# Kernel optimization log

Hardware: AMD Instinct MI355X
Metric: run time of the kernel (lower is better)

Reference implementation:

```python
import jax, jax.numpy as jnp
import numpy as np

ALPHA = 1.0   # get_spike_fn('ArcTan', 1.0, 20.0)
WIDTH = 20.0

@jax.custom_vjp
def arctan_spike(x):
    # Heaviside forward, ArcTan surrogate gradient
    return (x > 0).astype(x.dtype)

def _spike_fwd(x):
    return arctan_spike(x), x

def _spike_bwd(x, g):
    return (g * ALPHA / (1.0 + (WIDTH * x) ** 2),)

arctan_spike.defvjp(_spike_fwd, _spike_bwd)

T, B, F = 2048, 64, 512  # seq_len, batch, features (input_groups=256 -> F=512)
TAU_SYN, TAU_MEM, V_THRESH, W_SCALE = 0.08, 0.03, 1.0, 0.4

def setup_inputs() -> dict:
    key = jax.random.key(0)
    x = jax.random.normal(key, (T, B, F), dtype=jnp.float32)
    # ff weight: block_diag of input_groups copies of 0.4*I2 == 0.4*I_F
    W = (W_SCALE * jnp.eye(F, dtype=jnp.float32))
    leak_i = jnp.full((F,), 1.0 - TAU_SYN, dtype=jnp.float32)
    leak_v = jnp.full((F,), 1.0 - TAU_MEM, dtype=jnp.float32)
    thresh = jnp.full((F,), V_THRESH, dtype=jnp.float32)
    return {"x": x, "W": W, "leak_i": leak_i, "leak_v": leak_v, "thresh": thresh}

def reference(x, W, leak_i, leak_v, thresh):
    Tn, Bn, Fn = x.shape
    i0 = jnp.zeros((Bn, Fn), dtype=x.dtype)
    v0 = jnp.zeros((Bn, Fn), dtype=x.dtype)
    z0 = jnp.zeros((Bn, Fn), dtype=x.dtype)

    def step(carry, xt):
        i, v, z = carry
        ff = xt @ W.T                      # [B,F] linear synapse (no bias)
        i_new = leak_i * i + ff            # leaky synaptic current
        v_new = leak_v * v * (1.0 - z) + i_new  # membrane, reset-to-zero on spike
        z_new = arctan_spike(v_new - thresh)
        return (i_new, v_new, z_new), z_new

    _, out = jax.lax.scan(step, (i0, v0, z0), x)
    return out  # [T, B, F]
```

## Files before the change

### kernel.cpp

```cpp
#include <hip/hip_runtime.h>


typedef float v2f __attribute__((ext_vector_type(2)));
typedef float v4f __attribute__((ext_vector_type(4)));

constexpr int T_STEPS = 2048;
constexpr int B_DIM   = 64;
constexpr int F_DIM   = 512;
constexpr int BF      = B_DIM * F_DIM;
constexpr int BLK_FLOATS = 128;
constexpr int NBLK    = BF / BLK_FLOATS;
constexpr int CHUNK   = 64;
constexpr int NCHUNK  = T_STEPS / CHUNK;
constexpr int NPROD   = 4;
constexpr int STEPS_PER_PROD = CHUNK / NPROD;
constexpr int LOADS_PER_PROD = STEPS_PER_PROD / 2;
constexpr int LDS_FLOATS = 2 * CHUNK * BLK_FLOATS;

__global__ __launch_bounds__(320, 1) void snn_scan_kernel(
    const float* __restrict__ x,
    const float* __restrict__ W,
    const float* __restrict__ leak_i,
    const float* __restrict__ leak_v,
    const float* __restrict__ thresh,
    float* __restrict__ out) {

    __shared__ float lds[LDS_FLOATS];

    const int tid  = threadIdx.x;
    const int wid  = tid >> 6;
    const int lane = tid & 63;
    const int blk  = blockIdx.x;
    const bool is_prod = (wid < NPROD);

    const int  half = lane >> 5;
    const int  l32  = lane & 31;
    const int  sbase = wid * STEPS_PER_PROD + half;
    const float* xsrc = x + (size_t)blk * BLK_FLOATS + (size_t)l32 * 4;

    const int e  = blk * BLK_FLOATS + lane * 2;
    const int f0 = e & (F_DIM - 1);
    float w00 = 0.f, w01 = 0.f, w10 = 0.f, w11 = 0.f;
    float li0 = 0.f, li1 = 0.f, lv0 = 0.f, lv1 = 0.f, th0 = 0.f, th1 = 0.f;
    if (!is_prod) {
        w00 = W[(size_t)(f0    ) * F_DIM + f0    ];
        w01 = W[(size_t)(f0    ) * F_DIM + f0 + 1];
        w10 = W[(size_t)(f0 + 1) * F_DIM + f0    ];
        w11 = W[(size_t)(f0 + 1) * F_DIM + f0 + 1];
        li0 = leak_i[f0]; li1 = leak_i[f0 + 1];
        lv0 = leak_v[f0]; lv1 = leak_v[f0 + 1];
        th0 = thresh[f0]; th1 = thresh[f0 + 1];
    }
    float i0 = 0.f, v0 = 0.f, z0 = 0.f;
    float i1 = 0.f, v1 = 0.f, z1 = 0.f;
    float* osrc = out + e;

    auto produce = [&](int c) {
        const int db = c & 1;
        const float* gb = xsrc + (size_t)(c * CHUNK + sbase) * BF;
        v4f r[LOADS_PER_PROD];
        #pragma unroll
        for (int i = 0; i < LOADS_PER_PROD; ++i)
            r[i] = __builtin_nontemporal_load(
                       (const v4f*)(gb + (size_t)(2 * i) * BF));
        float* lb = &lds[(size_t)db * (CHUNK * BLK_FLOATS)
                         + (size_t)sbase * BLK_FLOATS + (size_t)l32 * 4];
        #pragma unroll
        for (int i = 0; i < LOADS_PER_PROD; ++i)
            *(v4f*)(lb + (size_t)(2 * i) * BLK_FLOATS) = r[i];
    };

    auto consume = [&](int c) {
        const int db = c & 1;
        const float* lb = &lds[(size_t)db * (CHUNK * BLK_FLOATS) + (size_t)lane * 2];
        float* ob = osrc + (size_t)c * CHUNK * BF;
        #pragma unroll 8
        for (int j = 0; j < CHUNK; ++j) {
            const v2f xv = *(const v2f*)(lb + (size_t)j * BLK_FLOATS);
            const float xe = xv.x;
            const float xo = xv.y;
            const float ff0 = __fadd_rn(__fmul_rn(w00, xe), __fmul_rn(w01, xo));
            const float ff1 = __fadd_rn(__fmul_rn(w10, xe), __fmul_rn(w11, xo));
            i0 = __fadd_rn(__fmul_rn(li0, i0), ff0);
            i1 = __fadd_rn(__fmul_rn(li1, i1), ff1);
            float vm0 = __fmul_rn(lv0, v0);
            float vm1 = __fmul_rn(lv1, v1);
            vm0 = (z0 > 0.0f) ? 0.0f : vm0;
            vm1 = (z1 > 0.0f) ? 0.0f : vm1;
            v0 = __fadd_rn(vm0, i0);
            v1 = __fadd_rn(vm1, i1);
            z0 = (v0 > th0) ? 1.0f : 0.0f;
            z1 = (v1 > th1) ? 1.0f : 0.0f;
            v2f zv; zv.x = z0; zv.y = z1;
            __builtin_nontemporal_store(zv, (v2f*)(ob + (size_t)j * BF));
        }
    };

    if (is_prod) produce(0);
    __syncthreads();

    for (int c = 0; c < NCHUNK; ++c) {
        if (is_prod) {
            if (c + 1 < NCHUNK) produce(c + 1);
        } else {
            consume(c);
        }
        __syncthreads();
    }
}

extern "C" void kernel_launch(void* const* d_in, const int* in_sizes, int n_in,
                              void* d_out, int out_size, void* d_ws, size_t ws_size,
                              hipStream_t stream) {
    const float* x      = (const float*)d_in[0];
    const float* W      = (const float*)d_in[1];
    const float* leak_i = (const float*)d_in[2];
    const float* leak_v = (const float*)d_in[3];
    const float* thresh = (const float*)d_in[4];
    float* out = (float*)d_out;

    snn_scan_kernel<<<dim3(NBLK), dim3(320), 0, stream>>>(
        x, W, leak_i, leak_v, thresh, out);
}
```

Measured before the change: 425.5 us.

## Stage consumer outputs through LDS and let producer waves write them out

The consumer wave now writes spike outputs into a double-buffered LDS output tile instead of storing directly to global memory. The producer waves copy the previous chunk's outputs from LDS to global with 16-byte nontemporal stores, alongside prefetching the next input chunk. This takes global store issue and latency off the serial recurrence wave and widens the store granularity. It doubles LDS use and adds more producer work per chunk, which could lengthen the producer phase.

```diff
diff --git a/kernel.cpp b/kernel.cpp
--- a/kernel.cpp
+++ b/kernel.cpp
@@ -15,7 +15,7 @@
 constexpr int NPROD   = 4;
 constexpr int STEPS_PER_PROD = CHUNK / NPROD;
 constexpr int LOADS_PER_PROD = STEPS_PER_PROD / 2;
-constexpr int LDS_FLOATS = 2 * CHUNK * BLK_FLOATS;
+constexpr int BUF_FLOATS = CHUNK * BLK_FLOATS;
 
 __global__ __launch_bounds__(320, 1) void snn_scan_kernel(
     const float* __restrict__ x,
@@ -25,7 +25,8 @@
     const float* __restrict__ thresh,
     float* __restrict__ out) {
 
-    __shared__ float lds[LDS_FLOATS];
+    __shared__ __attribute__((aligned(16))) float lds_x[2][BUF_FLOATS];
+    __shared__ __attribute__((aligned(16))) float lds_o[2][BUF_FLOATS];
 
     const int tid  = threadIdx.x;
     const int wid  = tid >> 6;
@@ -36,7 +37,8 @@
     const int  half = lane >> 5;
     const int  l32  = lane & 31;
     const int  sbase = wid * STEPS_PER_PROD + half;
-    const float* xsrc = x + (size_t)blk * BLK_FLOATS + (size_t)l32 * 4;
+    const float* xsrc = x   + (size_t)blk * BLK_FLOATS + (size_t)l32 * 4;
+    float*       odst = out + (size_t)blk * BLK_FLOATS + (size_t)l32 * 4;
 
     const int e  = blk * BLK_FLOATS + lane * 2;
     const int f0 = e & (F_DIM - 1);
@@ -53,7 +55,6 @@
     }
     float i0 = 0.f, v0 = 0.f, z0 = 0.f;
     float i1 = 0.f, v1 = 0.f, z1 = 0.f;
-    float* osrc = out + e;
 
     auto produce = [&](int c) {
         const int db = c & 1;
@@ -63,17 +64,29 @@
         for (int i = 0; i < LOADS_PER_PROD; ++i)
             r[i] = __builtin_nontemporal_load(
                        (const v4f*)(gb + (size_t)(2 * i) * BF));
-        float* lb = &lds[(size_t)db * (CHUNK * BLK_FLOATS)
-                         + (size_t)sbase * BLK_FLOATS + (size_t)l32 * 4];
+        float* lb = &lds_x[db][(size_t)sbase * BLK_FLOATS + (size_t)l32 * 4];
         #pragma unroll
         for (int i = 0; i < LOADS_PER_PROD; ++i)
             *(v4f*)(lb + (size_t)(2 * i) * BLK_FLOATS) = r[i];
     };
 
+    auto store_out = [&](int c) {
+        const int db = c & 1;
+        const float* lb = &lds_o[db][(size_t)sbase * BLK_FLOATS + (size_t)l32 * 4];
+        float* gb = odst + (size_t)(c * CHUNK + sbase) * BF;
+        v4f r[LOADS_PER_PROD];
+        #pragma unroll
+        for (int i = 0; i < LOADS_PER_PROD; ++i)
+            r[i] = *(const v4f*)(lb + (size_t)(2 * i) * BLK_FLOATS);
+        #pragma unroll
+        for (int i = 0; i < LOADS_PER_PROD; ++i)
+            __builtin_nontemporal_store(r[i], (v4f*)(gb + (size_t)(2 * i) * BF));
+    };
+
     auto consume = [&](int c) {
         const int db = c & 1;
-        const float* lb = &lds[(size_t)db * (CHUNK * BLK_FLOATS) + (size_t)lane * 2];
-        float* ob = osrc + (size_t)c * CHUNK * BF;
+        const float* lb = &lds_x[db][(size_t)lane * 2];
+        float*       lo = &lds_o[db][(size_t)lane * 2];
         #pragma unroll 8
         for (int j = 0; j < CHUNK; ++j) {
             const v2f xv = *(const v2f*)(lb + (size_t)j * BLK_FLOATS);
@@ -92,7 +105,7 @@
             z0 = (v0 > th0) ? 1.0f : 0.0f;
             z1 = (v1 > th1) ? 1.0f : 0.0f;
             v2f zv; zv.x = z0; zv.y = z1;
-            __builtin_nontemporal_store(zv, (v2f*)(ob + (size_t)j * BF));
+            *(v2f*)(lo + (size_t)j * BLK_FLOATS) = zv;
         }
     };
 
@@ -102,11 +115,13 @@
     for (int c = 0; c < NCHUNK; ++c) {
         if (is_prod) {
             if (c + 1 < NCHUNK) produce(c + 1);
+            if (c > 0) store_out(c - 1);
         } else {
             consume(c);
         }
         __syncthreads();
     }
+    if (is_prod) store_out(NCHUNK - 1);
 }
 
 extern "C" void kernel_launch(void* const* d_in, const int* in_sizes, int n_in,
```

New measurement: 426.7 us. Within noise of the previous version (+0.3%).
